# Kernel optimization log

Measured on AMD Instinct MI355X. Metric: run time of the kernel, lower is better.

Reference implementation:

```python
import jax, jax.numpy as jnp
import numpy as np

N_RES = 4096
N_PAIRS = 500000

def setup_inputs() -> dict:
    key = jax.random.key(0)
    k1, k2, k3 = jax.random.split(key, 3)
    ca_coords = jax.random.normal(k1, (N_RES, 3), dtype=jnp.float32) * 10.0
    K = jax.random.uniform(k2, (N_RES, N_RES), dtype=jnp.float32)
    pairs = jax.random.randint(k3, (N_PAIRS, 2), 0, N_RES, dtype=jnp.int64)
    return {"ca_coords": ca_coords, "K": K, "pairs": pairs}


def _reconstruct_backbone(ca):
    # vectorized version of reconstruct_backbone_atoms
    n = ca.shape[0]
    vec = ca[1:] - ca[:-1]                                  # (n-1,3)
    unit = vec / (jnp.linalg.norm(vec, axis=-1, keepdims=True) + 1e-8)
    # N atoms: n_coords[i] = ca[i] - 0.38*unit(ca[i]-ca[i-1]); n_coords[0] uses unit[0]
    n_coords = jnp.concatenate([ca[:1] - 0.38 * unit[:1], ca[1:] - 0.38 * unit], axis=0)
    # C atoms: c_coords[i] = ca[i] + 0.38*unit(ca[i+1]-ca[i]); c_coords[-1] uses unit[-1]
    c_coords = jnp.concatenate([ca[:-1] + 0.38 * unit, ca[-1:] + 0.38 * unit[-1:]], axis=0)
    # O atoms: perpendicular to (C-CA, N-CA) plane, last residue special-cased
    vec_n = n_coords[:-1] - ca[:-1]
    vec_c = c_coords[:-1] - ca[:-1]
    perp = jnp.cross(vec_c, vec_n)
    pnorm = jnp.linalg.norm(perp, axis=-1, keepdims=True)
    perp = jnp.where(pnorm > 1e-6, perp / jnp.maximum(pnorm, 1e-12), perp)
    o_body = c_coords[:-1] + 1.24 * perp
    o_last = c_coords[-1:] + jnp.array([[0.0, 1.24, 0.0]], dtype=ca.dtype)
    o_coords = jnp.concatenate([o_body, o_last], axis=0)
    return n_coords, c_coords, o_coords


def _pairwise_dist(x, y):
    # safe cdist: sqrt clamped so diagonal zeros stay differentiable
    sq = jnp.sum((x[:, None, :] - y[None, :, :]) ** 2, axis=-1)
    return jnp.sqrt(jnp.maximum(sq, 1e-12))


def reference(ca_coords, K, pairs):
    n = ca_coords.shape[0]

    # --- bond energy (weight=30): mean((|ca[i+1]-ca[i]| - 3.8)^2) ---
    d_bond = jnp.linalg.norm(ca_coords[1:] - ca_coords[:-1], axis=-1)
    e_bond = 30.0 * jnp.mean((d_bond - 3.8) ** 2)

    # --- clash energy (weight=50): mean(relu(3.2 - d_pair)^2) ---
    dv = ca_coords[pairs[:, 0]] - ca_coords[pairs[:, 1]]
    d_pair = jnp.sqrt(jnp.maximum(jnp.sum(dv ** 2, axis=-1), 1e-12))
    e_clash = 50.0 * jnp.mean(jax.nn.relu(3.2 - d_pair) ** 2)

    # --- contact energy (weight=5): mean((D - 8*(1-K))^2) over full NxN ---
    D = _pairwise_dist(ca_coords, ca_coords)
    target = 8.0 * (1.0 - K)
    e_contact = 5.0 * jnp.mean((D - target) ** 2)

    # --- hydrogen bond energy (weight=4) from reconstructed backbone ---
    n_coords, c_coords, o_coords = _reconstruct_backbone(ca_coords)
    ideal = 2.95
    hb = jnp.float32(0.0)
    # double loop i, j in [i+2, i+6) -> offsets 2..5, vectorized per offset
    for off in (2, 3, 4, 5):
        d = jnp.linalg.norm(o_coords[: n - off] - n_coords[off:], axis=-1)
        pen = jnp.exp(-(((d - ideal) / 0.3) ** 2))
        hb = hb - 0.5 * jnp.sum(jnp.where((d > 2.5) & (d < 3.5), pen, 0.0))
    e_hb = 4.0 * hb / (n * n)

    return e_bond + e_clash + e_contact + e_hb
```

## Files before the change

kernel.cpp:

```cpp
#include <hip/hip_runtime.h>
#include <math.h>

#define NRES 4096
#define ROWS 8
#define COLS 2048
#define NBLK ((NRES / ROWS) * (NRES / COLS))
#define HB_BLOCKS (NRES / 256)

__device__ __forceinline__ float wave_sum(float v) {
#pragma unroll
    for (int off = 32; off > 0; off >>= 1) v += __shfl_down(v, off, 64);
    return v;
}

__device__ __forceinline__ float c4(float4 kv, float4 cx, float4 cy, float4 cz,
                                    float xi, float yi, float zi, float s) {
    float dx, dy, dz, sq, D, t;
    dx = xi - cx.x; dy = yi - cy.x; dz = zi - cz.x;
    sq = fmaf(dx, dx, fmaf(dy, dy, dz * dz));
    D  = sqrtf(sq);
    t  = fmaf(8.f, kv.x, D - 8.f);
    s  = fmaf(t, t, s);

    dx = xi - cx.y; dy = yi - cy.y; dz = zi - cz.y;
    sq = fmaf(dx, dx, fmaf(dy, dy, dz * dz));
    D  = sqrtf(sq);
    t  = fmaf(8.f, kv.y, D - 8.f);
    s  = fmaf(t, t, s);

    dx = xi - cx.z; dy = yi - cy.z; dz = zi - cz.z;
    sq = fmaf(dx, dx, fmaf(dy, dy, dz * dz));
    D  = sqrtf(sq);
    t  = fmaf(8.f, kv.z, D - 8.f);
    s  = fmaf(t, t, s);

    dx = xi - cx.w; dy = yi - cy.w; dz = zi - cz.w;
    sq = fmaf(dx, dx, fmaf(dy, dy, dz * dz));
    D  = sqrtf(sq);
    t  = fmaf(8.f, kv.w, D - 8.f);
    s  = fmaf(t, t, s);
    return s;
}

__global__ __launch_bounds__(256, 4) void energy_kernel(const float* __restrict__ ca,
                                                        const float* __restrict__ K,
                                                        const int* __restrict__ pairs,
                                                        float4* __restrict__ partial,
                                                        int npairs) {
    __shared__ float sx[COLS], sy[COLS], sz[COLS];
    __shared__ float red[4][4];
    const int tid  = threadIdx.x;
    const int b    = blockIdx.x;
    const int tile = b & 1;
    const int row0 = (b >> 1) * ROWS;
    const int c0   = tile * COLS;

    for (int j = tid; j < COLS; j += 256) {
        int g = c0 + j;
        sx[j] = ca[3 * g + 0];
        sy[j] = ca[3 * g + 1];
        sz[j] = ca[3 * g + 2];
    }
    __syncthreads();

    float xi[ROWS], yi[ROWS], zi[ROWS];
#pragma unroll
    for (int r = 0; r < ROWS; ++r) {
        int g = row0 + r;
        xi[r] = ca[3 * g + 0];
        yi[r] = ca[3 * g + 1];
        zi[r] = ca[3 * g + 2];
    }

    const float* Kb = K + (size_t)row0 * NRES + c0;
    const int j0 = tid << 2;
    const int j1 = (tid + 256) << 2;
    float contact = 0.f;

    float4 va[4], vb[4];
#pragma unroll
    for (int r = 0; r < 4; ++r) va[r] = *(const float4*)(Kb + (size_t)r * NRES + j0);
#pragma unroll
    for (int r = 0; r < 4; ++r) vb[r] = *(const float4*)(Kb + (size_t)(4 + r) * NRES + j0);

    float4 cx0 = *(const float4*)&sx[j0];
    float4 cy0 = *(const float4*)&sy[j0];
    float4 cz0 = *(const float4*)&sz[j0];

#pragma unroll
    for (int r = 0; r < 4; ++r) contact = c4(va[r], cx0, cy0, cz0, xi[r], yi[r], zi[r], contact);
#pragma unroll
    for (int r = 0; r < 4; ++r) va[r] = *(const float4*)(Kb + (size_t)r * NRES + j1);
#pragma unroll
    for (int r = 0; r < 4; ++r) contact = c4(vb[r], cx0, cy0, cz0, xi[4 + r], yi[4 + r], zi[4 + r], contact);
#pragma unroll
    for (int r = 0; r < 4; ++r) vb[r] = *(const float4*)(Kb + (size_t)(4 + r) * NRES + j1);

    float4 cx1 = *(const float4*)&sx[j1];
    float4 cy1 = *(const float4*)&sy[j1];
    float4 cz1 = *(const float4*)&sz[j1];

#pragma unroll
    for (int r = 0; r < 4; ++r) contact = c4(va[r], cx1, cy1, cz1, xi[r], yi[r], zi[r], contact);
#pragma unroll
    for (int r = 0; r < 4; ++r) contact = c4(vb[r], cx1, cy1, cz1, xi[4 + r], yi[4 + r], zi[4 + r], contact);

    float clash = 0.f;
    for (int p = b * 256 + tid; p < npairs; p += NBLK * 256) {
        int2 pr = ((const int2*)pairs)[p];
        float dx = ca[3 * pr.x + 0] - ca[3 * pr.y + 0];
        float dy = ca[3 * pr.x + 1] - ca[3 * pr.y + 1];
        float dz = ca[3 * pr.x + 2] - ca[3 * pr.y + 2];
        float d  = sqrtf(fmaxf(fmaf(dx, dx, fmaf(dy, dy, dz * dz)), 1e-12f));
        float r  = fmaxf(3.2f - d, 0.f);
        clash = fmaf(r, r, clash);
    }

    float bond = 0.f, hb = 0.f;
    if (b < HB_BLOCKS) {
        const int i = b * 256 + tid;
        const int n = NRES;

        if (i < n - 1) {
            float dx = ca[3*(i+1)+0] - ca[3*i+0];
            float dy = ca[3*(i+1)+1] - ca[3*i+1];
            float dz = ca[3*(i+1)+2] - ca[3*i+2];
            float d  = sqrtf(fmaf(dx, dx, fmaf(dy, dy, dz * dz)));
            float t  = d - 3.8f;
            bond = t * t;
        }

        if (i < n - 2) {
            float cax = ca[3*i+0], cay = ca[3*i+1], caz = ca[3*i+2];
            float vx = ca[3*(i+1)+0] - cax, vy = ca[3*(i+1)+1] - cay, vz = ca[3*(i+1)+2] - caz;
            float inv = 1.f / (sqrtf(vx*vx + vy*vy + vz*vz) + 1e-8f);
            float ux = vx*inv, uy = vy*inv, uz = vz*inv;

            float upx, upy, upz;
            if (i == 0) { upx = ux; upy = uy; upz = uz; }
            else {
                float wx = cax - ca[3*(i-1)+0], wy = cay - ca[3*(i-1)+1], wz = caz - ca[3*(i-1)+2];
                float inv2 = 1.f / (sqrtf(wx*wx + wy*wy + wz*wz) + 1e-8f);
                upx = wx*inv2; upy = wy*inv2; upz = wz*inv2;
            }

            float vcx = 0.38f*ux,  vcy = 0.38f*uy,  vcz = 0.38f*uz;
            float vnx = -0.38f*upx, vny = -0.38f*upy, vnz = -0.38f*upz;
            float px = vcy*vnz - vcz*vny;
            float py = vcz*vnx - vcx*vnz;
            float pz = vcx*vny - vcy*vnx;
            float pn = sqrtf(px*px + py*py + pz*pz);
            if (pn > 1e-6f) {
                float ipn = 1.f / fmaxf(pn, 1e-12f);
                px *= ipn; py *= ipn; pz *= ipn;
            }
            float ox = cax + vcx + 1.24f*px;
            float oy = cay + vcy + 1.24f*py;
            float oz = caz + vcz + 1.24f*pz;

#pragma unroll
            for (int off = 2; off <= 5; ++off) {
                int jj = i + off;
                if (jj < n) {
                    float cjx = ca[3*jj+0], cjy = ca[3*jj+1], cjz = ca[3*jj+2];
                    float qx = cjx - ca[3*(jj-1)+0], qy = cjy - ca[3*(jj-1)+1], qz = cjz - ca[3*(jj-1)+2];
                    float invq = 1.f / (sqrtf(qx*qx + qy*qy + qz*qz) + 1e-8f);
                    float njx = cjx - 0.38f*qx*invq;
                    float njy = cjy - 0.38f*qy*invq;
                    float njz = cjz - 0.38f*qz*invq;
                    float ddx = ox-njx, ddy = oy-njy, ddz = oz-njz;
                    float d = sqrtf(ddx*ddx + ddy*ddy + ddz*ddz);
                    if (d > 2.5f && d < 3.5f) {
                        float z = (d - 2.95f) * (1.0f / 0.3f);
                        hb -= 0.5f * expf(-z*z);
                    }
                }
            }
        }
    }

    float vbo = wave_sum(bond);
    float vcl = wave_sum(clash);
    float vco = wave_sum(contact);
    float vhb = wave_sum(hb);
    const int wave = tid >> 6;
    if ((tid & 63) == 0) {
        red[wave][0] = vbo; red[wave][1] = vcl; red[wave][2] = vco; red[wave][3] = vhb;
    }
    __syncthreads();
    if (tid == 0) {
        float4 o;
        o.x = red[0][0] + red[1][0] + red[2][0] + red[3][0];
        o.y = red[0][1] + red[1][1] + red[2][1] + red[3][1];
        o.z = red[0][2] + red[1][2] + red[2][2] + red[3][2];
        o.w = red[0][3] + red[1][3] + red[2][3] + red[3][3];
        partial[b] = o;
    }
}

__global__ __launch_bounds__(256) void finalize_kernel(const float4* __restrict__ partial,
                                                       float* __restrict__ out,
                                                       int n, int npairs) {
    __shared__ float red[4][4];
    const int tid = threadIdx.x;
    float vb = 0.f, vc = 0.f, vk = 0.f, vh = 0.f;
#pragma unroll
    for (int s = 0; s < NBLK; s += 256) {
        float4 a = partial[tid + s];
        vb += a.x; vc += a.y; vk += a.z; vh += a.w;
    }
    vb = wave_sum(vb); vc = wave_sum(vc); vk = wave_sum(vk); vh = wave_sum(vh);
    const int wave = tid >> 6;
    if ((tid & 63) == 0) {
        red[wave][0] = vb; red[wave][1] = vc; red[wave][2] = vk; red[wave][3] = vh;
    }
    __syncthreads();
    if (tid == 0) {
        float bond    = red[0][0] + red[1][0] + red[2][0] + red[3][0];
        float clash   = red[0][1] + red[1][1] + red[2][1] + red[3][1];
        float contact = red[0][2] + red[1][2] + red[2][2] + red[3][2];
        float hb      = red[0][3] + red[1][3] + red[2][3] + red[3][3];
        float inv_nn  = 1.f / ((float)n * (float)n);
        out[0] = 30.f * bond / (float)(n - 1)
               + 50.f * clash / (float)npairs
               + 5.f  * contact * inv_nn
               + 4.f  * hb * inv_nn;
    }
}

extern "C" void kernel_launch(void* const* d_in, const int* in_sizes, int n_in,
                              void* d_out, int out_size, void* d_ws, size_t ws_size,
                              hipStream_t stream) {
    const float* ca    = (const float*)d_in[0];
    const float* K     = (const float*)d_in[1];
    const int*   pairs = (const int*)d_in[2];
    float* out = (float*)d_out;
    float4* partial = (float4*)d_ws;

    int n      = in_sizes[0] / 3;
    int npairs = in_sizes[2] / 2;

    energy_kernel<<<NBLK, 256, 0, stream>>>(ca, K, pairs, partial, npairs);
    finalize_kernel<<<1, 256, 0, stream>>>(partial, out, n, npairs);
}
```

Measured before the change: 109.0 us.

## Use persistent grid with full coords in LDS and double-buffered K row tiles

Replaces the 1024-block grid with a 768-block persistent grid. Each block loads all 4096 CA coordinates into LDS once, then loops over 4-row tiles of K, double-buffering float4 loads across four 1024-column chunks. Clash, bond and H-bond lookups now read coordinates from LDS instead of global gathers, and a raw hardware sqrt replaces sqrtf. The trade-off is 48KB of LDS per block, which limits occupancy (launch bounds drop to 3), and uneven tile counts per block (1024 tiles over 768 blocks).

New measurement: 101.3 us. -7.0%, faster.

```diff
diff --git a/kernel.cpp b/kernel.cpp
--- a/kernel.cpp
+++ b/kernel.cpp
@@ -1,10 +1,10 @@
 #include <hip/hip_runtime.h>
 #include <math.h>
 
-#define NRES 4096
-#define ROWS 8
-#define COLS 2048
-#define NBLK ((NRES / ROWS) * (NRES / COLS))
+#define NRES   4096
+#define GRID   768
+#define TROWS  4
+#define NTILES (NRES / TROWS)
 #define HB_BLOCKS (NRES / 256)
 
 __device__ __forceinline__ float wave_sum(float v) {
@@ -13,105 +13,93 @@
     return v;
 }
 
+__device__ __forceinline__ float fsqrt(float x) { return __builtin_amdgcn_sqrtf(x); }
+
 __device__ __forceinline__ float c4(float4 kv, float4 cx, float4 cy, float4 cz,
                                     float xi, float yi, float zi, float s) {
-    float dx, dy, dz, sq, D, t;
+    float dx, dy, dz, D, t;
     dx = xi - cx.x; dy = yi - cy.x; dz = zi - cz.x;
-    sq = fmaf(dx, dx, fmaf(dy, dy, dz * dz));
-    D  = sqrtf(sq);
+    D  = fsqrt(fmaf(dx, dx, fmaf(dy, dy, dz * dz)));
     t  = fmaf(8.f, kv.x, D - 8.f);
     s  = fmaf(t, t, s);
 
     dx = xi - cx.y; dy = yi - cy.y; dz = zi - cz.y;
-    sq = fmaf(dx, dx, fmaf(dy, dy, dz * dz));
-    D  = sqrtf(sq);
+    D  = fsqrt(fmaf(dx, dx, fmaf(dy, dy, dz * dz)));
     t  = fmaf(8.f, kv.y, D - 8.f);
     s  = fmaf(t, t, s);
 
     dx = xi - cx.z; dy = yi - cy.z; dz = zi - cz.z;
-    sq = fmaf(dx, dx, fmaf(dy, dy, dz * dz));
-    D  = sqrtf(sq);
+    D  = fsqrt(fmaf(dx, dx, fmaf(dy, dy, dz * dz)));
     t  = fmaf(8.f, kv.z, D - 8.f);
     s  = fmaf(t, t, s);
 
     dx = xi - cx.w; dy = yi - cy.w; dz = zi - cz.w;
-    sq = fmaf(dx, dx, fmaf(dy, dy, dz * dz));
-    D  = sqrtf(sq);
+    D  = fsqrt(fmaf(dx, dx, fmaf(dy, dy, dz * dz)));
     t  = fmaf(8.f, kv.w, D - 8.f);
     s  = fmaf(t, t, s);
     return s;
 }
 
-__global__ __launch_bounds__(256, 4) void energy_kernel(const float* __restrict__ ca,
+__global__ __launch_bounds__(256, 3) void energy_kernel(const float* __restrict__ ca,
                                                         const float* __restrict__ K,
                                                         const int* __restrict__ pairs,
                                                         float4* __restrict__ partial,
                                                         int npairs) {
-    __shared__ float sx[COLS], sy[COLS], sz[COLS];
+    __shared__ float sx[NRES], sy[NRES], sz[NRES];
     __shared__ float red[4][4];
-    const int tid  = threadIdx.x;
-    const int b    = blockIdx.x;
-    const int tile = b & 1;
-    const int row0 = (b >> 1) * ROWS;
-    const int c0   = tile * COLS;
-
-    for (int j = tid; j < COLS; j += 256) {
-        int g = c0 + j;
-        sx[j] = ca[3 * g + 0];
-        sy[j] = ca[3 * g + 1];
-        sz[j] = ca[3 * g + 2];
+    const int tid = threadIdx.x;
+    const int b   = blockIdx.x;
+
+    for (int j = tid; j < NRES; j += 256) {
+        sx[j] = ca[3 * j + 0];
+        sy[j] = ca[3 * j + 1];
+        sz[j] = ca[3 * j + 2];
     }
     __syncthreads();
 
-    float xi[ROWS], yi[ROWS], zi[ROWS];
-#pragma unroll
-    for (int r = 0; r < ROWS; ++r) {
-        int g = row0 + r;
-        xi[r] = ca[3 * g + 0];
-        yi[r] = ca[3 * g + 1];
-        zi[r] = ca[3 * g + 2];
-    }
-
-    const float* Kb = K + (size_t)row0 * NRES + c0;
-    const int j0 = tid << 2;
-    const int j1 = (tid + 256) << 2;
     float contact = 0.f;
-
-    float4 va[4], vb[4];
-#pragma unroll
-    for (int r = 0; r < 4; ++r) va[r] = *(const float4*)(Kb + (size_t)r * NRES + j0);
-#pragma unroll
-    for (int r = 0; r < 4; ++r) vb[r] = *(const float4*)(Kb + (size_t)(4 + r) * NRES + j0);
-
-    float4 cx0 = *(const float4*)&sx[j0];
-    float4 cy0 = *(const float4*)&sy[j0];
-    float4 cz0 = *(const float4*)&sz[j0];
-
-#pragma unroll
-    for (int r = 0; r < 4; ++r) contact = c4(va[r], cx0, cy0, cz0, xi[r], yi[r], zi[r], contact);
-#pragma unroll
-    for (int r = 0; r < 4; ++r) va[r] = *(const float4*)(Kb + (size_t)r * NRES + j1);
-#pragma unroll
-    for (int r = 0; r < 4; ++r) contact = c4(vb[r], cx0, cy0, cz0, xi[4 + r], yi[4 + r], zi[4 + r], contact);
-#pragma unroll
-    for (int r = 0; r < 4; ++r) vb[r] = *(const float4*)(Kb + (size_t)(4 + r) * NRES + j1);
-
-    float4 cx1 = *(const float4*)&sx[j1];
-    float4 cy1 = *(const float4*)&sy[j1];
-    float4 cz1 = *(const float4*)&sz[j1];
-
-#pragma unroll
-    for (int r = 0; r < 4; ++r) contact = c4(va[r], cx1, cy1, cz1, xi[r], yi[r], zi[r], contact);
-#pragma unroll
-    for (int r = 0; r < 4; ++r) contact = c4(vb[r], cx1, cy1, cz1, xi[4 + r], yi[4 + r], zi[4 + r], contact);
+    for (int t = b; t < NTILES; t += GRID) {
+        const int rbase = t * TROWS;
+        float xi[TROWS], yi[TROWS], zi[TROWS];
+#pragma unroll
+        for (int r = 0; r < TROWS; ++r) {
+            xi[r] = sx[rbase + r]; yi[r] = sy[rbase + r]; zi[r] = sz[rbase + r];
+        }
+
+        const float* Kt = K + (size_t)rbase * NRES;
+        const int j0 = tid << 2;
+        float4 va[TROWS], vb[TROWS];
+#pragma unroll
+        for (int r = 0; r < TROWS; ++r)
+            va[r] = *(const float4*)(Kt + (size_t)r * NRES + j0);
+
+#pragma unroll
+        for (int c = 0; c < 4; ++c) {
+            const int jc = j0 + (c << 10);
+            float4* cur = (c & 1) ? vb : va;
+            float4* nxt = (c & 1) ? va : vb;
+            if (c < 3) {
+                const int jn = j0 + ((c + 1) << 10);
+#pragma unroll
+                for (int r = 0; r < TROWS; ++r)
+                    nxt[r] = *(const float4*)(Kt + (size_t)r * NRES + jn);
+            }
+            const float4 cx = *(const float4*)&sx[jc];
+            const float4 cy = *(const float4*)&sy[jc];
+            const float4 cz = *(const float4*)&sz[jc];
+#pragma unroll
+            for (int r = 0; r < TROWS; ++r)
+                contact = c4(cur[r], cx, cy, cz, xi[r], yi[r], zi[r], contact);
+        }
+    }
 
     float clash = 0.f;
-    for (int p = b * 256 + tid; p < npairs; p += NBLK * 256) {
+    for (int p = b * 256 + tid; p < npairs; p += GRID * 256) {
         int2 pr = ((const int2*)pairs)[p];
-        float dx = ca[3 * pr.x + 0] - ca[3 * pr.y + 0];
-        float dy = ca[3 * pr.x + 1] - ca[3 * pr.y + 1];
-        float dz = ca[3 * pr.x + 2] - ca[3 * pr.y + 2];
-        float d  = sqrtf(fmaxf(fmaf(dx, dx, fmaf(dy, dy, dz * dz)), 1e-12f));
+        float dx = sx[pr.x] - sx[pr.y];
+        float dy = sy[pr.x] - sy[pr.y];
+        float dz = sz[pr.x] - sz[pr.y];
+        float d  = fsqrt(fmaxf(fmaf(dx, dx, fmaf(dy, dy, dz * dz)), 1e-12f));
         float r  = fmaxf(3.2f - d, 0.f);
         clash = fmaf(r, r, clash);
     }
@@ -122,24 +110,22 @@
         const int n = NRES;
 
         if (i < n - 1) {
-            float dx = ca[3*(i+1)+0] - ca[3*i+0];
-            float dy = ca[3*(i+1)+1] - ca[3*i+1];
-            float dz = ca[3*(i+1)+2] - ca[3*i+2];
+            float dx = sx[i+1]-sx[i], dy = sy[i+1]-sy[i], dz = sz[i+1]-sz[i];
             float d  = sqrtf(fmaf(dx, dx, fmaf(dy, dy, dz * dz)));
             float t  = d - 3.8f;
             bond = t * t;
         }
 
         if (i < n - 2) {
-            float cax = ca[3*i+0], cay = ca[3*i+1], caz = ca[3*i+2];
-            float vx = ca[3*(i+1)+0] - cax, vy = ca[3*(i+1)+1] - cay, vz = ca[3*(i+1)+2] - caz;
+            float cax = sx[i], cay = sy[i], caz = sz[i];
+            float vx = sx[i+1]-cax, vy = sy[i+1]-cay, vz = sz[i+1]-caz;
             float inv = 1.f / (sqrtf(vx*vx + vy*vy + vz*vz) + 1e-8f);
             float ux = vx*inv, uy = vy*inv, uz = vz*inv;
 
             float upx, upy, upz;
             if (i == 0) { upx = ux; upy = uy; upz = uz; }
             else {
-                float wx = cax - ca[3*(i-1)+0], wy = cay - ca[3*(i-1)+1], wz = caz - ca[3*(i-1)+2];
+                float wx = cax-sx[i-1], wy = cay-sy[i-1], wz = caz-sz[i-1];
                 float inv2 = 1.f / (sqrtf(wx*wx + wy*wy + wz*wz) + 1e-8f);
                 upx = wx*inv2; upy = wy*inv2; upz = wz*inv2;
             }
@@ -162,8 +148,8 @@
             for (int off = 2; off <= 5; ++off) {
                 int jj = i + off;
                 if (jj < n) {
-                    float cjx = ca[3*jj+0], cjy = ca[3*jj+1], cjz = ca[3*jj+2];
-                    float qx = cjx - ca[3*(jj-1)+0], qy = cjy - ca[3*(jj-1)+1], qz = cjz - ca[3*(jj-1)+2];
+                    float cjx = sx[jj], cjy = sy[jj], cjz = sz[jj];
+                    float qx = cjx-sx[jj-1], qy = cjy-sy[jj-1], qz = cjz-sz[jj-1];
                     float invq = 1.f / (sqrtf(qx*qx + qy*qy + qz*qz) + 1e-8f);
                     float njx = cjx - 0.38f*qx*invq;
                     float njy = cjy - 0.38f*qy*invq;
@@ -205,7 +191,7 @@
     const int tid = threadIdx.x;
     float vb = 0.f, vc = 0.f, vk = 0.f, vh = 0.f;
 #pragma unroll
-    for (int s = 0; s < NBLK; s += 256) {
+    for (int s = 0; s < GRID; s += 256) {
         float4 a = partial[tid + s];
         vb += a.x; vc += a.y; vk += a.z; vh += a.w;
     }
@@ -240,6 +226,6 @@
     int n      = in_sizes[0] / 3;
     int npairs = in_sizes[2] / 2;
 
-    energy_kernel<<<NBLK, 256, 0, stream>>>(ca, K, pairs, partial, npairs);
+    energy_kernel<<<GRID, 256, 0, stream>>>(ca, K, pairs, partial, npairs);
     finalize_kernel<<<1, 256, 0, stream>>>(partial, out, n, npairs);
 }
```
